# Kernel tuning notes

Hardware: AMD Instinct MI355X
Metric: run time of the kernel (lower is better)

Reference implementation:

```python
import jax, jax.numpy as jnp
import numpy as np

N_NODES = 50000


def _gcn_norm(edge_index, num_nodes):
    # add self loops, compute symmetric normalization D^-1/2 (A+I) D^-1/2
    loops = jnp.arange(num_nodes, dtype=edge_index.dtype)
    row = jnp.concatenate([edge_index[0], loops])
    col = jnp.concatenate([edge_index[1], loops])
    deg = jax.ops.segment_sum(jnp.ones_like(row, dtype=jnp.float32), col,
                              num_segments=num_nodes)
    dinv = jnp.where(deg > 0, jax.lax.rsqrt(deg), 0.0)
    norm = dinv[row] * dinv[col]  # [E']
    return row, col, norm


def _gcn_conv(x, W, b, row, col, norm, num_nodes):
    h = x @ W                       # [N, out] transform first (smaller dim)
    msg = h[row] * norm[:, None]    # gather along source nodes  [E', out]
    agg = jax.ops.segment_sum(msg, col, num_segments=num_nodes)  # scatter-add
    return agg + b


def setup_inputs() -> dict:
    key = jax.random.key(0)
    k1, k2, k3, k4 = jax.random.split(key, 4)
    x = jax.random.normal(k1, (N_NODES, 128), dtype=jnp.float32)
    edge_index = jax.random.randint(k2, (2, 800000), 0, N_NODES, dtype=jnp.int64)
    W1 = jax.random.normal(k3, (128, 128), dtype=jnp.float32) * (1.0 / np.sqrt(128))
    b1 = jnp.zeros((128,), dtype=jnp.float32)
    W2 = jax.random.normal(k4, (128, 16), dtype=jnp.float32) * (1.0 / np.sqrt(128))
    b2 = jnp.zeros((16,), dtype=jnp.float32)
    return {"x": x, "edge_index": edge_index, "W1": W1, "b1": b1, "W2": W2, "b2": b2}


def reference(x, edge_index, W1, b1, W2, b2):
    n = x.shape[0]
    row, col, norm = _gcn_norm(edge_index, n)
    h = _gcn_conv(x, W1, b1, row, col, norm, n)
    h = jax.nn.relu(h)
    h = _gcn_conv(h, W2, b2, row, col, norm, n)
    return jax.nn.log_softmax(h, axis=1)
```

## Files before the change

kernel.cpp:

```cpp
#include <hip/hip_runtime.h>
#include <math.h>

constexpr int N  = 50000;
constexpr int E  = 800000;
constexpr int F1 = 128;
constexpr int F2 = 16;
constexpr int BSHIFT  = 8;
constexpr int NBUCKET = (N + 255) >> BSHIFT;
constexpr int CHUNK   = 2048;
constexpr int CAP     = 6144;

typedef unsigned short ushort_t;
typedef unsigned char  uchar_t;
typedef __bf16 bf16x8 __attribute__((ext_vector_type(8)));
typedef float  f32x4  __attribute__((ext_vector_type(4)));

static __device__ __forceinline__ float blo(unsigned u) { return __uint_as_float(u << 16); }
static __device__ __forceinline__ float bhi(unsigned u) { return __uint_as_float(u & 0xffff0000u); }
static __device__ __forceinline__ ushort_t to_bf(float f) { __bf16 h = (__bf16)f; return *(ushort_t*)&h; }
static __device__ __forceinline__ uchar_t to_fp8(float f) {
    return (uchar_t)(__builtin_amdgcn_cvt_pk_fp8_f32(f, f, 0, false) & 0xff);
}

__global__ __launch_bounds__(256) void k_scatterP(const int* __restrict__ row,
                                                  const int* __restrict__ col,
                                                  int* __restrict__ cursor,
                                                  unsigned* __restrict__ P,
                                                  const float* __restrict__ W1,
                                                  const float* __restrict__ W2,
                                                  ushort_t* __restrict__ W1t,
                                                  ushort_t* __restrict__ W2t) {
    __shared__ int hist[NBUCKET];
    __shared__ int cur[NBUCKET];
    int t = threadIdx.x;
    if (t < NBUCKET) hist[t] = 0;
    __syncthreads();
    int base = blockIdx.x * CHUNK;
#pragma unroll
    for (int i = 0; i < CHUNK / 256; ++i) {
        int e = base + i * 256 + t;
        if (e < E) atomicAdd(&hist[col[e] >> BSHIFT], 1);
    }
    __syncthreads();
    if (t < NBUCKET) cur[t] = t * CAP + atomicAdd(&cursor[t], hist[t]);
    __syncthreads();
#pragma unroll
    for (int i = 0; i < CHUNK / 256; ++i) {
        int e = base + i * 256 + t;
        if (e < E) {
            int c = col[e];
            int pos = atomicAdd(&cur[c >> BSHIFT], 1);
            P[pos] = ((unsigned)row[e] << BSHIFT) | (unsigned)(c & 255);
        }
    }

    int gi = blockIdx.x * 256 + t;
    if (gi < F1 * F1) {
        int k = gi >> 7, n = gi & 127;
        W1t[n * F1 + k] = to_bf(W1[gi]);
    }
    if (gi < F1 * F2) {
        int k = gi >> 4, n = gi & 15;
        W2t[n * F1 + k] = to_bf(W2[gi]);
    }
}

__global__ __launch_bounds__(512) void k_binFinal(const unsigned* __restrict__ P,
                                                  const int* __restrict__ cursor,
                                                  ushort_t* __restrict__ csr16,
                                                  int* __restrict__ seg_start,
                                                  int* __restrict__ counts,
                                                  float* __restrict__ dinv) {
    __shared__ unsigned eb[CAP];
    __shared__ int cnt[256];
    __shared__ int cur[256];
    __shared__ int wtot[4];
    int t = threadIdx.x;
    int b = blockIdx.x;
    int lo = b << BSHIFT;
    int n_nodes = min(256, N - lo);
    int m = cursor[b];
    if (t < 256) cnt[t] = 0;
    __syncthreads();
    const unsigned* Pb = P + (size_t)b * CAP;
    for (int k = t; k < m; k += 512) {
        unsigned u = Pb[k];
        eb[k] = u;
        atomicAdd(&cnt[u & 255], 1);
    }
    __syncthreads();
    int lane = t & 63, wid = t >> 6;
    int v = 0, incl = 0;
    if (t < 256) {
        v = cnt[t];
        incl = v;
#pragma unroll
        for (int d = 1; d < 64; d <<= 1) {
            int u = __shfl_up(incl, d, 64);
            if (lane >= d) incl += u;
        }
        if (lane == 63) wtot[wid] = incl;
    }
    __syncthreads();
    if (t < 256) {
        int wb = 0;
        for (int w = 0; w < wid; ++w) wb += wtot[w];
        int o = b * CAP + wb + incl - v;
        cur[t] = o;
        if (t < n_nodes) {
            seg_start[lo + t] = o;
            counts[lo + t] = v;
            dinv[lo + t] = rsqrtf((float)v + 1.f);
        }
    }
    __syncthreads();
    for (int k = t; k < m; k += 512) {
        unsigned u = eb[k];
        int pos = atomicAdd(&cur[u & 255], 1);
        csr16[pos] = (ushort_t)(u >> BSHIFT);
    }
}

__global__ __launch_bounds__(256) void k_gemm1_mfma(const float* __restrict__ x,
                                                    const ushort_t* __restrict__ W1t,
                                                    const float* __restrict__ dinv,
                                                    uchar_t* __restrict__ h1q) {
    __shared__ ushort_t Wl[F1 * 136];
    int t = threadIdx.x;
    for (int i = t; i < F1 * 16; i += 256) {
        int n = i >> 4, c = (i & 15) * 8;
        *(int4*)&Wl[n * 136 + c] = *(const int4*)&W1t[n * F1 + c];
    }
    __syncthreads();

    int lane = t & 63, wv = t >> 6;
    int quad = lane >> 4, l15 = lane & 15;
    int arow = blockIdx.x * 64 + wv * 16 + l15;
    int rclamp = min(arow, N - 1);
    f32x4 acc[8] = {};

#pragma unroll
    for (int kk = 0; kk < 4; ++kk) {
        int k0 = kk * 32 + quad * 8;
        const float* xp = x + (size_t)rclamp * F1 + k0;
        float4 u0 = *(const float4*)xp;
        float4 u1 = *(const float4*)(xp + 4);
        bf16x8 a;
        a[0] = (__bf16)u0.x; a[1] = (__bf16)u0.y; a[2] = (__bf16)u0.z; a[3] = (__bf16)u0.w;
        a[4] = (__bf16)u1.x; a[5] = (__bf16)u1.y; a[6] = (__bf16)u1.z; a[7] = (__bf16)u1.w;
#pragma unroll
        for (int ct = 0; ct < 8; ++ct) {
            bf16x8 b = *(const bf16x8*)&Wl[(ct * 16 + l15) * 136 + k0];
            acc[ct] = __builtin_amdgcn_mfma_f32_16x16x32_bf16(a, b, acc[ct], 0, 0, 0);
        }
    }

    int orow0 = blockIdx.x * 64 + wv * 16 + quad * 4;
#pragma unroll
    for (int r = 0; r < 4; ++r) {
        int orow = orow0 + r;
        if (orow < N) {
            float d = dinv[orow];
#pragma unroll
            for (int ct = 0; ct < 8; ++ct)
                h1q[(size_t)orow * F1 + ct * 16 + l15] = to_fp8(acc[ct][r] * d);
        }
    }
}

__global__ __launch_bounds__(256) void k_gather1(const uchar_t* __restrict__ h1q,
                                                 const int* __restrict__ seg_start,
                                                 const int* __restrict__ counts,
                                                 const ushort_t* __restrict__ csr16,
                                                 const float* __restrict__ dinv,
                                                 const float* __restrict__ b1,
                                                 ushort_t* __restrict__ h1rb) {
    int c = (blockIdx.x * 256 + threadIdx.x) >> 6;
    int lane = threadIdx.x & 63;
    if (c >= N) return;
    int s = seg_start[c], e = s + counts[c];
    float ax = 0.f, ay = 0.f;
    int k = s;
    for (; k + 4 <= e; k += 4) {
        int r0 = csr16[k], r1 = csr16[k + 1], r2 = csr16[k + 2], r3 = csr16[k + 3];
        unsigned u0 = ((const ushort_t*)(h1q + (size_t)r0 * F1))[lane];
        unsigned u1 = ((const ushort_t*)(h1q + (size_t)r1 * F1))[lane];
        unsigned u2 = ((const ushort_t*)(h1q + (size_t)r2 * F1))[lane];
        unsigned u3 = ((const ushort_t*)(h1q + (size_t)r3 * F1))[lane];
        ax += (__builtin_amdgcn_cvt_f32_fp8(u0, 0) + __builtin_amdgcn_cvt_f32_fp8(u1, 0)) +
              (__builtin_amdgcn_cvt_f32_fp8(u2, 0) + __builtin_amdgcn_cvt_f32_fp8(u3, 0));
        ay += (__builtin_amdgcn_cvt_f32_fp8(u0, 1) + __builtin_amdgcn_cvt_f32_fp8(u1, 1)) +
              (__builtin_amdgcn_cvt_f32_fp8(u2, 1) + __builtin_amdgcn_cvt_f32_fp8(u3, 1));
    }
    for (; k < e; ++k) {
        unsigned u = ((const ushort_t*)(h1q + (size_t)csr16[k] * F1))[lane];
        ax += __builtin_amdgcn_cvt_f32_fp8(u, 0);
        ay += __builtin_amdgcn_cvt_f32_fp8(u, 1);
    }
    unsigned us = ((const ushort_t*)(h1q + (size_t)c * F1))[lane];
    ax += __builtin_amdgcn_cvt_f32_fp8(us, 0);
    ay += __builtin_amdgcn_cvt_f32_fp8(us, 1);
    float dc = dinv[c];
    float2 bb = ((const float2*)b1)[lane];
    float o0 = fmaxf(fmaf(dc, ax, bb.x), 0.f);
    float o1 = fmaxf(fmaf(dc, ay, bb.y), 0.f);
    unsigned pw = (unsigned)to_bf(o0) | ((unsigned)to_bf(o1) << 16);
    ((unsigned*)(h1rb + (size_t)c * F1))[lane] = pw;
}

__global__ __launch_bounds__(256) void k_gemm2_mfma(const ushort_t* __restrict__ h1rb,
                                                    const ushort_t* __restrict__ W2t,
                                                    const float* __restrict__ dinv,
                                                    ushort_t* __restrict__ h2s) {
    int t = threadIdx.x, lane = t & 63, wv = t >> 6;
    int quad = lane >> 4, l15 = lane & 15;
    int arow = blockIdx.x * 64 + wv * 16 + l15;
    int rclamp = min(arow, N - 1);
    f32x4 acc = {};
#pragma unroll
    for (int kk = 0; kk < 4; ++kk) {
        int k0 = kk * 32 + quad * 8;
        bf16x8 a = *(const bf16x8*)(h1rb + (size_t)rclamp * F1 + k0);
        bf16x8 b = *(const bf16x8*)(W2t + l15 * F1 + k0);
        acc = __builtin_amdgcn_mfma_f32_16x16x32_bf16(a, b, acc, 0, 0, 0);
    }
    int orow0 = blockIdx.x * 64 + wv * 16 + quad * 4;
#pragma unroll
    for (int r = 0; r < 4; ++r) {
        int orow = orow0 + r;
        if (orow < N)
            h2s[(size_t)orow * F2 + l15] = to_bf(acc[r] * dinv[orow]);
    }
}

__global__ __launch_bounds__(256) void k_gather2(const ushort_t* __restrict__ h2s,
                                                 const int* __restrict__ seg_start,
                                                 const int* __restrict__ counts,
                                                 const ushort_t* __restrict__ csr16,
                                                 const float* __restrict__ dinv,
                                                 const float* __restrict__ b2,
                                                 float* __restrict__ out) {
    int idx = blockIdx.x * 256 + threadIdx.x;
    int node = idx >> 3, sub = idx & 7;
    if (node >= N) return;
    int s = seg_start[node], e = s + counts[node];
    float ax = 0.f, ay = 0.f;
    int k = s;
    for (; k + 4 <= e; k += 4) {
        int r0 = csr16[k], r1 = csr16[k + 1], r2 = csr16[k + 2], r3 = csr16[k + 3];
        unsigned u0 = ((const unsigned*)(h2s + (size_t)r0 * F2))[sub];
        unsigned u1 = ((const unsigned*)(h2s + (size_t)r1 * F2))[sub];
        unsigned u2 = ((const unsigned*)(h2s + (size_t)r2 * F2))[sub];
        unsigned u3 = ((const unsigned*)(h2s + (size_t)r3 * F2))[sub];
        ax += (blo(u0) + blo(u1)) + (blo(u2) + blo(u3));
        ay += (bhi(u0) + bhi(u1)) + (bhi(u2) + bhi(u3));
    }
    for (; k < e; ++k) {
        unsigned u = ((const unsigned*)(h2s + (size_t)csr16[k] * F2))[sub];
        ax += blo(u);
        ay += bhi(u);
    }
    unsigned us = ((const unsigned*)(h2s + (size_t)node * F2))[sub];
    ax += blo(us);
    ay += bhi(us);
    float dc = dinv[node];
    float2 bb = ((const float2*)b2)[sub];
    float v0 = fmaf(dc, ax, bb.x);
    float v1 = fmaf(dc, ay, bb.y);
    float mx = fmaxf(v0, v1);
#pragma unroll
    for (int m = 1; m < 8; m <<= 1) mx = fmaxf(mx, __shfl_xor(mx, m));
    float sm = expf(v0 - mx) + expf(v1 - mx);
#pragma unroll
    for (int m = 1; m < 8; m <<= 1) sm += __shfl_xor(sm, m);
    float lse = mx + logf(sm);
    float2 o;
    o.x = v0 - lse;
    o.y = v1 - lse;
    ((float2*)(out + (size_t)node * F2))[sub] = o;
}

extern "C" void kernel_launch(void* const* d_in, const int* in_sizes, int n_in,
                              void* d_out, int out_size, void* d_ws, size_t ws_size,
                              hipStream_t stream) {
    const float* x  = (const float*)d_in[0];
    const int*   ei = (const int*)d_in[1];
    const float* W1 = (const float*)d_in[2];
    const float* b1 = (const float*)d_in[3];
    const float* W2 = (const float*)d_in[4];
    const float* b2 = (const float*)d_in[5];
    const int* row = ei;
    const int* col = ei + E;

    char* ws = (char*)d_ws;
    int*      cursor    = (int*)ws;      ws += 256 * 4;
    unsigned* P         = (unsigned*)ws; ws += (size_t)NBUCKET * CAP * 4;
    ushort_t* csr16     = (ushort_t*)ws; ws += (size_t)NBUCKET * CAP * 2;
    int*      seg_start = (int*)ws;      ws += (size_t)N * 4;
    int*      counts    = (int*)ws;      ws += (size_t)N * 4;
    float*    dinv      = (float*)ws;    ws += (size_t)N * 4;
    ushort_t* W1t       = (ushort_t*)ws; ws += (size_t)F1 * F1 * 2;
    ushort_t* W2t       = (ushort_t*)ws; ws += (size_t)F2 * F1 * 2;
    uchar_t*  h1q       = (uchar_t*)ws;  ws += (size_t)N * F1;
    ushort_t* h1rb      = (ushort_t*)ws; ws += (size_t)N * F1 * 2;
    ushort_t* h2s       = (ushort_t*)ws; ws += (size_t)N * F2 * 2;

    hipMemsetAsync(cursor, 0, 256 * 4, stream);

    int nbin_blocks = (E + CHUNK - 1) / CHUNK;
    k_scatterP<<<nbin_blocks, 256, 0, stream>>>(row, col, cursor, P, W1, W2, W1t, W2t);
    k_binFinal<<<NBUCKET, 512, 0, stream>>>(P, cursor, csr16, seg_start, counts, dinv);

    k_gemm1_mfma<<<(N + 63) / 64, 256, 0, stream>>>(x, W1t, dinv, h1q);
    k_gather1<<<((size_t)N * 64 + 255) / 256, 256, 0, stream>>>(h1q, seg_start, counts, csr16,
                                                                dinv, b1, h1rb);

    k_gemm2_mfma<<<(N + 63) / 64, 256, 0, stream>>>(h1rb, W2t, dinv, h2s);
    k_gather2<<<((size_t)N * 8 + 255) / 256, 256, 0, stream>>>(h2s, seg_start, counts, csr16,
                                                               dinv, b2, (float*)d_out);
}
```

Baseline: 164.4 us.

## Permute h1 fp8 feature layout and gather four edges per wave in parallel

The GEMM1 epilogue now packs each lane's eight column-tile outputs into one 8-byte store, so h1 features are stored in a permuted order. W2t and b1 are permuted to match. The layer-1 gather now splits each wave into four 16-lane groups that handle four edges at once with 8-byte loads, then combines the groups with cross-lane shuffles. This aims to cut per-edge load instructions and loop trip count, at the cost of shuffle reductions and wasted lanes on the last partial set of edges.

```diff
diff --git a/kernel.cpp b/kernel.cpp
--- a/kernel.cpp
+++ b/kernel.cpp
@@ -18,9 +18,7 @@
 static __device__ __forceinline__ float blo(unsigned u) { return __uint_as_float(u << 16); }
 static __device__ __forceinline__ float bhi(unsigned u) { return __uint_as_float(u & 0xffff0000u); }
 static __device__ __forceinline__ ushort_t to_bf(float f) { __bf16 h = (__bf16)f; return *(ushort_t*)&h; }
-static __device__ __forceinline__ uchar_t to_fp8(float f) {
-    return (uchar_t)(__builtin_amdgcn_cvt_pk_fp8_f32(f, f, 0, false) & 0xff);
-}
+
 
 __global__ __launch_bounds__(256) void k_scatterP(const int* __restrict__ row,
                                                   const int* __restrict__ col,
@@ -28,8 +26,10 @@
                                                   unsigned* __restrict__ P,
                                                   const float* __restrict__ W1,
                                                   const float* __restrict__ W2,
+                                                  const float* __restrict__ b1,
                                                   ushort_t* __restrict__ W1t,
-                                                  ushort_t* __restrict__ W2t) {
+                                                  ushort_t* __restrict__ W2t,
+                                                  float* __restrict__ b1p) {
     __shared__ int hist[NBUCKET];
     __shared__ int cur[NBUCKET];
     int t = threadIdx.x;
@@ -61,7 +61,11 @@
     }
     if (gi < F1 * F2) {
         int k = gi >> 4, n = gi & 15;
-        W2t[n * F1 + k] = to_bf(W2[gi]);
+        int pk = (k & 15) * 8 + (k >> 4);
+        W2t[n * F1 + pk] = to_bf(W2[gi]);
+    }
+    if (gi < F1) {
+        b1p[(gi & 15) * 8 + (gi >> 4)] = b1[gi];
     }
 }
 
@@ -161,9 +165,12 @@
         int orow = orow0 + r;
         if (orow < N) {
             float d = dinv[orow];
-#pragma unroll
-            for (int ct = 0; ct < 8; ++ct)
-                h1q[(size_t)orow * F1 + ct * 16 + l15] = to_fp8(acc[ct][r] * d);
+            unsigned d0 = __builtin_amdgcn_cvt_pk_fp8_f32(acc[0][r] * d, acc[1][r] * d, 0, false);
+            d0 = __builtin_amdgcn_cvt_pk_fp8_f32(acc[2][r] * d, acc[3][r] * d, d0, true);
+            unsigned d1 = __builtin_amdgcn_cvt_pk_fp8_f32(acc[4][r] * d, acc[5][r] * d, 0, false);
+            d1 = __builtin_amdgcn_cvt_pk_fp8_f32(acc[6][r] * d, acc[7][r] * d, d1, true);
+            uint2 pw; pw.x = d0; pw.y = d1;
+            *(uint2*)(h1q + (size_t)orow * F1 + l15 * 8) = pw;
         }
     }
 }
@@ -173,39 +180,64 @@
                                                  const int* __restrict__ counts,
                                                  const ushort_t* __restrict__ csr16,
                                                  const float* __restrict__ dinv,
-                                                 const float* __restrict__ b1,
+                                                 const float* __restrict__ b1p,
                                                  ushort_t* __restrict__ h1rb) {
     int c = (blockIdx.x * 256 + threadIdx.x) >> 6;
     int lane = threadIdx.x & 63;
     if (c >= N) return;
+    int sub = lane & 15, q = lane >> 4;
     int s = seg_start[c], e = s + counts[c];
-    float ax = 0.f, ay = 0.f;
-    int k = s;
-    for (; k + 4 <= e; k += 4) {
-        int r0 = csr16[k], r1 = csr16[k + 1], r2 = csr16[k + 2], r3 = csr16[k + 3];
-        unsigned u0 = ((const ushort_t*)(h1q + (size_t)r0 * F1))[lane];
-        unsigned u1 = ((const ushort_t*)(h1q + (size_t)r1 * F1))[lane];
-        unsigned u2 = ((const ushort_t*)(h1q + (size_t)r2 * F1))[lane];
-        unsigned u3 = ((const ushort_t*)(h1q + (size_t)r3 * F1))[lane];
-        ax += (__builtin_amdgcn_cvt_f32_fp8(u0, 0) + __builtin_amdgcn_cvt_f32_fp8(u1, 0)) +
-              (__builtin_amdgcn_cvt_f32_fp8(u2, 0) + __builtin_amdgcn_cvt_f32_fp8(u3, 0));
-        ay += (__builtin_amdgcn_cvt_f32_fp8(u0, 1) + __builtin_amdgcn_cvt_f32_fp8(u1, 1)) +
-              (__builtin_amdgcn_cvt_f32_fp8(u2, 1) + __builtin_amdgcn_cvt_f32_fp8(u3, 1));
-    }
-    for (; k < e; ++k) {
-        unsigned u = ((const ushort_t*)(h1q + (size_t)csr16[k] * F1))[lane];
-        ax += __builtin_amdgcn_cvt_f32_fp8(u, 0);
-        ay += __builtin_amdgcn_cvt_f32_fp8(u, 1);
-    }
-    unsigned us = ((const ushort_t*)(h1q + (size_t)c * F1))[lane];
-    ax += __builtin_amdgcn_cvt_f32_fp8(us, 0);
-    ay += __builtin_amdgcn_cvt_f32_fp8(us, 1);
-    float dc = dinv[c];
-    float2 bb = ((const float2*)b1)[lane];
-    float o0 = fmaxf(fmaf(dc, ax, bb.x), 0.f);
-    float o1 = fmaxf(fmaf(dc, ay, bb.y), 0.f);
-    unsigned pw = (unsigned)to_bf(o0) | ((unsigned)to_bf(o1) << 16);
-    ((unsigned*)(h1rb + (size_t)c * F1))[lane] = pw;
+    float acc[8] = {0.f, 0.f, 0.f, 0.f, 0.f, 0.f, 0.f, 0.f};
+    for (int base = s; base < e; base += 4) {
+        int k = base + q;
+        bool valid = k < e;
+        int r = c;
+        if (valid) r = csr16[k];
+        uint2 u = *(const uint2*)(h1q + (size_t)r * F1 + sub * 8);
+        float w = valid ? 1.f : 0.f;
+        acc[0] = fmaf(__builtin_amdgcn_cvt_f32_fp8(u.x, 0), w, acc[0]);
+        acc[1] = fmaf(__builtin_amdgcn_cvt_f32_fp8(u.x, 1), w, acc[1]);
+        acc[2] = fmaf(__builtin_amdgcn_cvt_f32_fp8(u.x, 2), w, acc[2]);
+        acc[3] = fmaf(__builtin_amdgcn_cvt_f32_fp8(u.x, 3), w, acc[3]);
+        acc[4] = fmaf(__builtin_amdgcn_cvt_f32_fp8(u.y, 0), w, acc[4]);
+        acc[5] = fmaf(__builtin_amdgcn_cvt_f32_fp8(u.y, 1), w, acc[5]);
+        acc[6] = fmaf(__builtin_amdgcn_cvt_f32_fp8(u.y, 2), w, acc[6]);
+        acc[7] = fmaf(__builtin_amdgcn_cvt_f32_fp8(u.y, 3), w, acc[7]);
+    }
+    if (q == 0) {
+        uint2 u = *(const uint2*)(h1q + (size_t)c * F1 + sub * 8);
+        acc[0] += __builtin_amdgcn_cvt_f32_fp8(u.x, 0);
+        acc[1] += __builtin_amdgcn_cvt_f32_fp8(u.x, 1);
+        acc[2] += __builtin_amdgcn_cvt_f32_fp8(u.x, 2);
+        acc[3] += __builtin_amdgcn_cvt_f32_fp8(u.x, 3);
+        acc[4] += __builtin_amdgcn_cvt_f32_fp8(u.y, 0);
+        acc[5] += __builtin_amdgcn_cvt_f32_fp8(u.y, 1);
+        acc[6] += __builtin_amdgcn_cvt_f32_fp8(u.y, 2);
+        acc[7] += __builtin_amdgcn_cvt_f32_fp8(u.y, 3);
+    }
+#pragma unroll
+    for (int j = 0; j < 8; ++j) acc[j] += __shfl_xor(acc[j], 16);
+#pragma unroll
+    for (int j = 0; j < 8; ++j) acc[j] += __shfl_xor(acc[j], 32);
+    if (q == 0) {
+        float dc = dinv[c];
+        float4 bb0 = ((const float4*)b1p)[sub * 2];
+        float4 bb1 = ((const float4*)b1p)[sub * 2 + 1];
+        float o0 = fmaxf(fmaf(dc, acc[0], bb0.x), 0.f);
+        float o1 = fmaxf(fmaf(dc, acc[1], bb0.y), 0.f);
+        float o2 = fmaxf(fmaf(dc, acc[2], bb0.z), 0.f);
+        float o3 = fmaxf(fmaf(dc, acc[3], bb0.w), 0.f);
+        float o4 = fmaxf(fmaf(dc, acc[4], bb1.x), 0.f);
+        float o5 = fmaxf(fmaf(dc, acc[5], bb1.y), 0.f);
+        float o6 = fmaxf(fmaf(dc, acc[6], bb1.z), 0.f);
+        float o7 = fmaxf(fmaf(dc, acc[7], bb1.w), 0.f);
+        int4 pw;
+        pw.x = (int)((unsigned)to_bf(o0) | ((unsigned)to_bf(o1) << 16));
+        pw.y = (int)((unsigned)to_bf(o2) | ((unsigned)to_bf(o3) << 16));
+        pw.z = (int)((unsigned)to_bf(o4) | ((unsigned)to_bf(o5) << 16));
+        pw.w = (int)((unsigned)to_bf(o6) | ((unsigned)to_bf(o7) << 16));
+        *(int4*)(h1rb + (size_t)c * F1 + sub * 8) = pw;
+    }
 }
 
 __global__ __launch_bounds__(256) void k_gemm2_mfma(const ushort_t* __restrict__ h1rb,
@@ -295,10 +327,11 @@
     char* ws = (char*)d_ws;
     int*      cursor    = (int*)ws;      ws += 256 * 4;
     unsigned* P         = (unsigned*)ws; ws += (size_t)NBUCKET * CAP * 4;
-    ushort_t* csr16     = (ushort_t*)ws; ws += (size_t)NBUCKET * CAP * 2;
+    ushort_t* csr16     = (ushort_t*)ws; ws += (size_t)(NBUCKET * CAP + 8) * 2;
     int*      seg_start = (int*)ws;      ws += (size_t)N * 4;
     int*      counts    = (int*)ws;      ws += (size_t)N * 4;
     float*    dinv      = (float*)ws;    ws += (size_t)N * 4;
+    float*    b1p       = (float*)ws;    ws += (size_t)F1 * 4;
     ushort_t* W1t       = (ushort_t*)ws; ws += (size_t)F1 * F1 * 2;
     ushort_t* W2t       = (ushort_t*)ws; ws += (size_t)F2 * F1 * 2;
     uchar_t*  h1q       = (uchar_t*)ws;  ws += (size_t)N * F1;
@@ -308,12 +341,12 @@
     hipMemsetAsync(cursor, 0, 256 * 4, stream);
 
     int nbin_blocks = (E + CHUNK - 1) / CHUNK;
-    k_scatterP<<<nbin_blocks, 256, 0, stream>>>(row, col, cursor, P, W1, W2, W1t, W2t);
+    k_scatterP<<<nbin_blocks, 256, 0, stream>>>(row, col, cursor, P, W1, W2, b1, W1t, W2t, b1p);
     k_binFinal<<<NBUCKET, 512, 0, stream>>>(P, cursor, csr16, seg_start, counts, dinv);
 
     k_gemm1_mfma<<<(N + 63) / 64, 256, 0, stream>>>(x, W1t, dinv, h1q);
     k_gather1<<<((size_t)N * 64 + 255) / 256, 256, 0, stream>>>(h1q, seg_start, counts, csr16,
-                                                                dinv, b1, h1rb);
+                                                                dinv, b1p, h1rb);
 
     k_gemm2_mfma<<<(N + 63) / 64, 256, 0, stream>>>(h1rb, W2t, dinv, h2s);
     k_gather2<<<((size_t)N * 8 + 255) / 256, 256, 0, stream>>>(h2s, seg_start, counts, csr16,
```

After: 166.0 us. Within noise of the previous version (+1.0%).
